# Kernel tuning notes

Measured on AMD Instinct MI355X. Metric: run time of the kernel, lower is better.

## Reference

```python
import jax, jax.numpy as jnp
import numpy as np

B, H, P, L = 16, 128, 64, 8192  # batch, d_input, d_state, seq_len
TWO_PI = 6.283185307179586


def setup_inputs() -> dict:
    key = jax.random.key(0)
    k_u, k_lr, k_li, k_br, k_bi, k_cr, k_ci, k_d = jax.random.split(key, 8)
    u = jax.random.normal(k_u, (B, H, L), dtype=jnp.float32)
    # continuous-time diagonal state matrix: Lambda = -rand + i*2*pi*rand
    lam_re = -jax.random.uniform(k_lr, (P,), dtype=jnp.float32)
    lam_im = TWO_PI * jax.random.uniform(k_li, (P,), dtype=jnp.float32)
    Lam = lam_re + 1j * lam_im                       # (P,) complex64
    Lambda_bar = jnp.exp(Lam)                        # ZOH with Delta=1
    # continuous B, then ZOH: B_bar = (Lambda_bar - 1)/Lambda * B
    Bc = (jax.random.normal(k_br, (P, H), dtype=jnp.float32)
          + 1j * jax.random.normal(k_bi, (P, H), dtype=jnp.float32))
    B_bar = ((Lambda_bar - 1.0) / Lam)[:, None] * Bc  # (P,H) complex64
    C = (jax.random.normal(k_cr, (H, P), dtype=jnp.float32)
         + 1j * jax.random.normal(k_ci, (H, P), dtype=jnp.float32))
    D = jax.random.normal(k_d, (H, H), dtype=jnp.float32)
    return {
        "u": u,
        "Lambda_re": jnp.real(Lambda_bar).astype(jnp.float32),
        "Lambda_im": jnp.imag(Lambda_bar).astype(jnp.float32),
        "B_re": jnp.real(B_bar).astype(jnp.float32),
        "B_im": jnp.imag(B_bar).astype(jnp.float32),
        "C_re": jnp.real(C).astype(jnp.float32),
        "C_im": jnp.imag(C).astype(jnp.float32),
        "D": D,
    }


def _binary_op(elem_i, elem_j):
    # diagonal linear recurrence combine: (A^i, Bu_i) o (A^j, Bu_j)
    a_i, bu_i = elem_i
    a_j, bu_j = elem_j
    return a_j * a_i, a_j * bu_i + bu_j


def reference(u, Lambda_re, Lambda_im, B_re, B_im, C_re, C_im, D):
    Lambda_bar = Lambda_re + 1j * Lambda_im           # (P,)
    B_bar = B_re + 1j * B_im                          # (P,H)
    C = C_re + 1j * C_im                              # (H,P)
    uc = u.astype(B_bar.dtype)                        # (B,H,L) complex
    Bu = jnp.einsum('ph,bhl->bpl', B_bar, uc)         # (B,P,L)
    A = jnp.broadcast_to(Lambda_bar[None, :, None], Bu.shape)
    # parallel associative scan of the diagonal linear recurrence over L
    _, xs = jax.lax.associative_scan(_binary_op, (A, Bu), axis=2)  # (B,P,L)
    C_A_Bu = jnp.einsum('hp,bpl->bhl', C, xs).real    # (B,H,L)
    # einsum('hh,bhl->bhl', D, u) uses only the diagonal of D
    Du = jnp.diagonal(D)[None, :, None] * u           # (B,H,L)
    return jax.nn.gelu(C_A_Bu + Du, approximate=False)
```

## Files before the change

### kernel.cpp

```cpp
#include <hip/hip_runtime.h>
#include <math.h>

#define NB 16
#define NH 128
#define NP 64
#define NL 8192
#define NCHUNK 64

__global__ __launch_bounds__(256) void k_bu_scan(
    const float* __restrict__ u, const float* __restrict__ Bre,
    const float* __restrict__ Bim, const float* __restrict__ Lre,
    const float* __restrict__ Lim, float2* __restrict__ xloc,
    float2* __restrict__ Echunk) {
  __shared__ __align__(16) float sBre[32][68];
  __shared__ float sBim[32][68];
  __shared__ float sU[32][128];
  const int b  = blockIdx.y;
  const int c  = blockIdx.x;
  const int l0 = c * 128;
  const int t  = threadIdx.x;
  const int tp = t & 15;
  const int tl = t >> 4;
  float accRe[4][8], accIm[4][8];
  #pragma unroll
  for (int i = 0; i < 4; ++i)
    #pragma unroll
    for (int j = 0; j < 8; ++j) { accRe[i][j] = 0.f; accIm[i][j] = 0.f; }

  for (int ht = 0; ht < 4; ++ht) {
    const int h0 = ht * 32;
    #pragma unroll
    for (int idx = t; idx < 2048; idx += 256) {
      int h = idx & 31, p = idx >> 5;
      sBre[h][p] = Bre[p * NH + h0 + h];
      sBim[h][p] = Bim[p * NH + h0 + h];
    }
    #pragma unroll
    for (int idx = t; idx < 32 * 128; idx += 256) {
      int l = idx & 127, h = idx >> 7;
      sU[h][l] = u[((size_t)(b * NH + h0 + h)) * NL + l0 + l];
    }
    __syncthreads();
    #pragma unroll 4
    for (int h = 0; h < 32; ++h) {
      float4 br4 = *(const float4*)&sBre[h][tp * 4];
      float4 bi4 = *(const float4*)&sBim[h][tp * 4];
      float4 ua  = *(const float4*)&sU[h][tl * 8];
      float4 ub  = *(const float4*)&sU[h][tl * 8 + 4];
      float uu[8] = {ua.x, ua.y, ua.z, ua.w, ub.x, ub.y, ub.z, ub.w};
      float brr[4] = {br4.x, br4.y, br4.z, br4.w};
      float bii[4] = {bi4.x, bi4.y, bi4.z, bi4.w};
      #pragma unroll
      for (int i = 0; i < 4; ++i)
        #pragma unroll
        for (int j = 0; j < 8; ++j) {
          accRe[i][j] = fmaf(brr[i], uu[j], accRe[i][j]);
          accIm[i][j] = fmaf(bii[i], uu[j], accIm[i][j]);
        }
    }
    __syncthreads();
  }

  float lr[4], li[4];
  #pragma unroll
  for (int i = 0; i < 4; ++i) { lr[i] = Lre[tp * 4 + i]; li[i] = Lim[tp * 4 + i]; }
  #pragma unroll
  for (int i = 0; i < 4; ++i) {
    float xr = 0.f, xi = 0.f;
    #pragma unroll
    for (int j = 0; j < 8; ++j) {
      float nr = fmaf(lr[i], xr, fmaf(-li[i], xi, accRe[i][j]));
      float ni = fmaf(lr[i], xi, fmaf( li[i], xr, accIm[i][j]));
      xr = nr; xi = ni; accRe[i][j] = xr; accIm[i][j] = xi;
    }
  }

  float2* E = reinterpret_cast<float2*>(&sBre[0][0]);
  #define EL(p, q) E[(p) * 17 + (q)]
  #pragma unroll
  for (int i = 0; i < 4; ++i)
    EL(tp * 4 + i, tl) = make_float2(accRe[i][7], accIm[i][7]);

  float wr[4], wi[4];
  #pragma unroll
  for (int i = 0; i < 4; ++i) {
    float ar = lr[i], ai = li[i];
    #pragma unroll
    for (int k = 0; k < 3; ++k) { float nr = ar * ar - ai * ai; ai = 2.f * ar * ai; ar = nr; }
    wr[i] = ar; wi[i] = ai;
  }
  __syncthreads();
  #pragma unroll
  for (int d = 1; d < 16; d <<= 1) {
    float2 rv[4];
    #pragma unroll
    for (int i = 0; i < 4; ++i)
      rv[i] = (tl >= d) ? EL(tp * 4 + i, tl - d) : make_float2(0.f, 0.f);
    __syncthreads();
    if (tl >= d) {
      #pragma unroll
      for (int i = 0; i < 4; ++i) {
        float2 cur = EL(tp * 4 + i, tl);
        cur.x += wr[i] * rv[i].x - wi[i] * rv[i].y;
        cur.y += wr[i] * rv[i].y + wi[i] * rv[i].x;
        EL(tp * 4 + i, tl) = cur;
      }
    }
    __syncthreads();
    #pragma unroll
    for (int i = 0; i < 4; ++i) {
      float nr = wr[i] * wr[i] - wi[i] * wi[i];
      wi[i] = 2.f * wr[i] * wi[i]; wr[i] = nr;
    }
  }

  float2 cin[4];
  #pragma unroll
  for (int i = 0; i < 4; ++i)
    cin[i] = (tl > 0) ? EL(tp * 4 + i, tl - 1) : make_float2(0.f, 0.f);
  if (t < 64) {
    float2 tot = EL(t, 15);
    Echunk[((size_t)(b * NCHUNK + c)) * NP + t] = tot;
  }

  #pragma unroll
  for (int i = 0; i < 4; ++i) {
    float cr = cin[i].x, ci = cin[i].y;
    #pragma unroll
    for (int j = 0; j < 8; ++j) {
      float nr = lr[i] * cr - li[i] * ci;
      float nc = lr[i] * ci + li[i] * cr;
      cr = nr; ci = nc;
      accRe[i][j] += cr; accIm[i][j] += ci;
    }
  }

  #pragma unroll
  for (int i = 0; i < 4; ++i) {
    size_t base = ((size_t)(b * NP + tp * 4 + i)) * NL + l0 + tl * 8;
    #pragma unroll
    for (int j = 0; j < 8; j += 2) {
      float4 v = make_float4(accRe[i][j], accIm[i][j], accRe[i][j + 1], accIm[i][j + 1]);
      *(float4*)&xloc[base + j] = v;
    }
  }
  #undef EL
}

__global__ __launch_bounds__(64) void k_carry(
    const float2* __restrict__ Echunk, const float* __restrict__ Lre,
    const float* __restrict__ Lim, float2* __restrict__ carryg,
    float2* __restrict__ powtab) {
  const int p = blockIdx.x;
  const int b = blockIdx.y;
  const int t = threadIdx.x;
  const float lr = Lre[p], li = Lim[p];
  float wr = lr, wi = li;
  #pragma unroll
  for (int k = 0; k < 7; ++k) { float nr = wr * wr - wi * wi; wi = 2.f * wr * wi; wr = nr; }
  float2 e = Echunk[((size_t)(b * NCHUNK + t)) * NP + p];
  float sr = e.x, si = e.y;
  float fr = wr, fi = wi;
  #pragma unroll
  for (int d = 1; d < 64; d <<= 1) {
    float pr = __shfl_up(sr, d);
    float pi = __shfl_up(si, d);
    if (t >= d) { sr += fr * pr - fi * pi; si += fr * pi + fi * pr; }
    float nr = fr * fr - fi * fi; fi = 2.f * fr * fi; fr = nr;
  }
  float cr = __shfl_up(sr, 1);
  float ci = __shfl_up(si, 1);
  if (t == 0) { cr = 0.f; ci = 0.f; }
  carryg[((size_t)(b * NCHUNK + t)) * NP + p] = make_float2(cr, ci);

  if (b == 0) {
    float ar = lr, ai = li, br = 1.f, bi = 0.f;
    int e1 = t + 1;
    while (e1) {
      if (e1 & 1) { float nr = br * ar - bi * ai; bi = br * ai + bi * ar; br = nr; }
      float nr = ar * ar - ai * ai; ai = 2.f * ar * ai; ar = nr;
      e1 >>= 1;
    }
    powtab[p * 128 + t] = make_float2(br, bi);
    float qr = lr, qi = li;
    #pragma unroll
    for (int k = 0; k < 6; ++k) { float nr = qr * qr - qi * qi; qi = 2.f * qr * qi; qr = nr; }
    float hr = br * qr - bi * qi, hi = br * qi + bi * qr;
    powtab[p * 128 + t + 64] = make_float2(hr, hi);
  }
}

__global__ __launch_bounds__(256) void k_out(
    const float2* __restrict__ xs, const float* __restrict__ u,
    const float* __restrict__ Cre, const float* __restrict__ Cim,
    const float* __restrict__ D, const float2* __restrict__ carryg,
    const float2* __restrict__ powtab, float* __restrict__ out) {
  __shared__ float sCre[16][132];
  __shared__ float sCim[16][132];
  __shared__ float sXre[16][128];
  __shared__ float sXim[16][128];
  __shared__ float sDd[128];
  const int b  = blockIdx.y;
  const int c  = blockIdx.x;
  const int l0 = c * 128;
  const int t  = threadIdx.x;
  const int lane = t & 63, w = t >> 6;
  const int th = (lane & 7) + 8 * (w & 1);
  const int tl = (lane >> 3) + 8 * (w >> 1);
  const int lfix = t & 127;
  const int ppb  = t >> 7;

  if (t < 128) sDd[t] = D[t * NH + t];

  float acc[8][8];
  #pragma unroll
  for (int i = 0; i < 8; ++i)
    #pragma unroll
    for (int j = 0; j < 8; ++j) acc[i][j] = 0.f;

  float2 gx[8], gp[8], gc[8];
  #pragma unroll
  for (int k = 0; k < 8; ++k) {
    int pp = ppb + 2 * k;
    gx[k] = xs[((size_t)(b * NP + pp)) * NL + l0 + lfix];
    gp[k] = powtab[pp * 128 + lfix];
    gc[k] = carryg[((size_t)(b * NCHUNK + c)) * NP + pp];
  }

  #pragma unroll
  for (int pt = 0; pt < 4; ++pt) {
    const int p0 = pt * 16;
    __syncthreads();
    #pragma unroll
    for (int idx = t; idx < 2048; idx += 256) {
      int pp = idx & 15, h = idx >> 4;
      sCre[pp][h] = Cre[h * NP + p0 + pp];
      sCim[pp][h] = Cim[h * NP + p0 + pp];
    }
    #pragma unroll
    for (int k = 0; k < 8; ++k) {
      int pp = ppb + 2 * k;
      float xr = gx[k].x + gp[k].x * gc[k].x - gp[k].y * gc[k].y;
      float xi = gx[k].y + gp[k].x * gc[k].y + gp[k].y * gc[k].x;
      sXre[pp][lfix] = xr; sXim[pp][lfix] = xi;
    }
    __syncthreads();
    if (pt < 3) {
      const int p1 = (pt + 1) * 16;
      #pragma unroll
      for (int k = 0; k < 8; ++k) {
        int pp = ppb + 2 * k;
        gx[k] = xs[((size_t)(b * NP + p1 + pp)) * NL + l0 + lfix];
        gp[k] = powtab[(p1 + pp) * 128 + lfix];
        gc[k] = carryg[((size_t)(b * NCHUNK + c)) * NP + p1 + pp];
      }
    }
    #pragma unroll 4
    for (int pp = 0; pp < 16; ++pp) {
      float4 ca = *(const float4*)&sCre[pp][th * 8];
      float4 cb = *(const float4*)&sCre[pp][th * 8 + 4];
      float4 ia = *(const float4*)&sCim[pp][th * 8];
      float4 ib = *(const float4*)&sCim[pp][th * 8 + 4];
      float4 xa = *(const float4*)&sXre[pp][tl * 8];
      float4 xb = *(const float4*)&sXre[pp][tl * 8 + 4];
      float4 ya = *(const float4*)&sXim[pp][tl * 8];
      float4 yb = *(const float4*)&sXim[pp][tl * 8 + 4];
      float cr[8] = {ca.x, ca.y, ca.z, ca.w, cb.x, cb.y, cb.z, cb.w};
      float ci[8] = {ia.x, ia.y, ia.z, ia.w, ib.x, ib.y, ib.z, ib.w};
      float xr[8] = {xa.x, xa.y, xa.z, xa.w, xb.x, xb.y, xb.z, xb.w};
      float xi[8] = {ya.x, ya.y, ya.z, ya.w, yb.x, yb.y, yb.z, yb.w};
      #pragma unroll
      for (int i = 0; i < 8; ++i)
        #pragma unroll
        for (int j = 0; j < 8; ++j) {
          acc[i][j] = fmaf(cr[i], xr[j], acc[i][j]);
          acc[i][j] = fmaf(-ci[i], xi[j], acc[i][j]);
        }
    }
  }

  #pragma unroll
  for (int i = 0; i < 8; ++i) {
    const int h = th * 8 + i;
    const float dd = sDd[h];
    size_t rb = ((size_t)(b * NH + h)) * NL + l0 + tl * 8;
    float4 u0 = *(const float4*)&u[rb];
    float4 u1 = *(const float4*)&u[rb + 4];
    float uu[8] = {u0.x, u0.y, u0.z, u0.w, u1.x, u1.y, u1.z, u1.w};
    float r[8];
    #pragma unroll
    for (int j = 0; j < 8; ++j) {
      float vv = acc[i][j] + dd * uu[j];
      r[j] = 0.5f * vv * (1.0f + erff(vv * 0.70710678118654752f));
    }
    *(float4*)&out[rb]     = make_float4(r[0], r[1], r[2], r[3]);
    *(float4*)&out[rb + 4] = make_float4(r[4], r[5], r[6], r[7]);
  }
}

extern "C" void kernel_launch(void* const* d_in, const int* in_sizes, int n_in,
                              void* d_out, int out_size, void* d_ws, size_t ws_size,
                              hipStream_t stream) {
  (void)in_sizes; (void)n_in; (void)out_size; (void)ws_size;
  const float* u   = (const float*)d_in[0];
  const float* Lre = (const float*)d_in[1];
  const float* Lim = (const float*)d_in[2];
  const float* Bre = (const float*)d_in[3];
  const float* Bim = (const float*)d_in[4];
  const float* Cre = (const float*)d_in[5];
  const float* Cim = (const float*)d_in[6];
  const float* Dm  = (const float*)d_in[7];
  float* out = (float*)d_out;

  char* wsb = (char*)d_ws;
  float2* xloc   = (float2*)wsb;
  float2* Echunk = (float2*)(wsb + 67108864);
  float2* carryg = (float2*)(wsb + 67108864 + 524288);
  float2* powtab = (float2*)(wsb + 67108864 + 1048576);

  dim3 g(NL / 128, NB);
  k_bu_scan<<<g, 256, 0, stream>>>(u, Bre, Bim, Lre, Lim, xloc, Echunk);
  dim3 gc(NP, NB);
  k_carry<<<gc, 64, 0, stream>>>(Echunk, Lre, Lim, carryg, powtab);
  k_out<<<g, 256, 0, stream>>>(xloc, u, Cre, Cim, Dm, carryg, powtab, out);
}
```

Baseline: 259.5 us.

## Rewrite output projection kernel with bf16 MFMA and smaller L tiles

Replaces the scalar-FMA complex C·x projection in the output kernel with bf16 MFMA 16x16x32 instructions. C (real and negated imaginary parts) and the carry-corrected states are converted to bf16 and staged in shared memory, and the L tile shrinks to 64 so there are twice as many blocks. The goal is to move the dominant GEMM onto the matrix cores. The cost is lower precision in the projection, plus per-block reconversion of the full C matrix. The epilogue now does scalar, non-vectorised loads of u and stores to out.

```diff
diff --git a/kernel.cpp b/kernel.cpp
--- a/kernel.cpp
+++ b/kernel.cpp
@@ -6,6 +6,13 @@
 #define NP 64
 #define NL 8192
 #define NCHUNK 64
+
+typedef __attribute__((ext_vector_type(8))) short bf16x8;
+typedef __attribute__((ext_vector_type(4))) float f32x4;
+
+__device__ __forceinline__ unsigned toBF(unsigned u) {
+  return (u + 0x7FFFu + ((u >> 16) & 1u)) >> 16;
+}
 
 __global__ __launch_bounds__(256) void k_bu_scan(
     const float* __restrict__ u, const float* __restrict__ Bre,
@@ -190,111 +197,74 @@
   }
 }
 
-__global__ __launch_bounds__(256) void k_out(
+__global__ __launch_bounds__(256) void k_out_mfma(
     const float2* __restrict__ xs, const float* __restrict__ u,
     const float* __restrict__ Cre, const float* __restrict__ Cim,
     const float* __restrict__ D, const float2* __restrict__ carryg,
     const float2* __restrict__ powtab, float* __restrict__ out) {
-  __shared__ float sCre[16][132];
-  __shared__ float sCim[16][132];
-  __shared__ float sXre[16][128];
-  __shared__ float sXim[16][128];
+  __shared__ __align__(16) unsigned short Asl[128][136];
+  __shared__ __align__(16) unsigned short Bsl[64][136];
   __shared__ float sDd[128];
   const int b  = blockIdx.y;
-  const int c  = blockIdx.x;
-  const int l0 = c * 128;
+  const int l0 = blockIdx.x * 64;
   const int t  = threadIdx.x;
   const int lane = t & 63, w = t >> 6;
-  const int th = (lane & 7) + 8 * (w & 1);
-  const int tl = (lane >> 3) + 8 * (w >> 1);
-  const int lfix = t & 127;
-  const int ppb  = t >> 7;
 
   if (t < 128) sDd[t] = D[t * NH + t];
 
-  float acc[8][8];
-  #pragma unroll
-  for (int i = 0; i < 8; ++i)
-    #pragma unroll
-    for (int j = 0; j < 8; ++j) acc[i][j] = 0.f;
-
-  float2 gx[8], gp[8], gc[8];
-  #pragma unroll
-  for (int k = 0; k < 8; ++k) {
-    int pp = ppb + 2 * k;
-    gx[k] = xs[((size_t)(b * NP + pp)) * NL + l0 + lfix];
-    gp[k] = powtab[pp * 128 + lfix];
-    gc[k] = carryg[((size_t)(b * NCHUNK + c)) * NP + pp];
-  }
-
-  #pragma unroll
-  for (int pt = 0; pt < 4; ++pt) {
-    const int p0 = pt * 16;
-    __syncthreads();
-    #pragma unroll
-    for (int idx = t; idx < 2048; idx += 256) {
-      int pp = idx & 15, h = idx >> 4;
-      sCre[pp][h] = Cre[h * NP + p0 + pp];
-      sCim[pp][h] = Cim[h * NP + p0 + pp];
-    }
-    #pragma unroll
-    for (int k = 0; k < 8; ++k) {
-      int pp = ppb + 2 * k;
-      float xr = gx[k].x + gp[k].x * gc[k].x - gp[k].y * gc[k].y;
-      float xi = gx[k].y + gp[k].x * gc[k].y + gp[k].y * gc[k].x;
-      sXre[pp][lfix] = xr; sXim[pp][lfix] = xi;
-    }
-    __syncthreads();
-    if (pt < 3) {
-      const int p1 = (pt + 1) * 16;
-      #pragma unroll
-      for (int k = 0; k < 8; ++k) {
-        int pp = ppb + 2 * k;
-        gx[k] = xs[((size_t)(b * NP + p1 + pp)) * NL + l0 + lfix];
-        gp[k] = powtab[(p1 + pp) * 128 + lfix];
-        gc[k] = carryg[((size_t)(b * NCHUNK + c)) * NP + p1 + pp];
-      }
-    }
-    #pragma unroll 4
-    for (int pp = 0; pp < 16; ++pp) {
-      float4 ca = *(const float4*)&sCre[pp][th * 8];
-      float4 cb = *(const float4*)&sCre[pp][th * 8 + 4];
-      float4 ia = *(const float4*)&sCim[pp][th * 8];
-      float4 ib = *(const float4*)&sCim[pp][th * 8 + 4];
-      float4 xa = *(const float4*)&sXre[pp][tl * 8];
-      float4 xb = *(const float4*)&sXre[pp][tl * 8 + 4];
-      float4 ya = *(const float4*)&sXim[pp][tl * 8];
-      float4 yb = *(const float4*)&sXim[pp][tl * 8 + 4];
-      float cr[8] = {ca.x, ca.y, ca.z, ca.w, cb.x, cb.y, cb.z, cb.w};
-      float ci[8] = {ia.x, ia.y, ia.z, ia.w, ib.x, ib.y, ib.z, ib.w};
-      float xr[8] = {xa.x, xa.y, xa.z, xa.w, xb.x, xb.y, xb.z, xb.w};
-      float xi[8] = {ya.x, ya.y, ya.z, ya.w, yb.x, yb.y, yb.z, yb.w};
-      #pragma unroll
-      for (int i = 0; i < 8; ++i)
-        #pragma unroll
-        for (int j = 0; j < 8; ++j) {
-          acc[i][j] = fmaf(cr[i], xr[j], acc[i][j]);
-          acc[i][j] = fmaf(-ci[i], xi[j], acc[i][j]);
-        }
-    }
-  }
-
-  #pragma unroll
-  for (int i = 0; i < 8; ++i) {
-    const int h = th * 8 + i;
-    const float dd = sDd[h];
-    size_t rb = ((size_t)(b * NH + h)) * NL + l0 + tl * 8;
-    float4 u0 = *(const float4*)&u[rb];
-    float4 u1 = *(const float4*)&u[rb + 4];
-    float uu[8] = {u0.x, u0.y, u0.z, u0.w, u1.x, u1.y, u1.z, u1.w};
-    float r[8];
-    #pragma unroll
-    for (int j = 0; j < 8; ++j) {
-      float vv = acc[i][j] + dd * uu[j];
-      r[j] = 0.5f * vv * (1.0f + erff(vv * 0.70710678118654752f));
-    }
-    *(float4*)&out[rb]     = make_float4(r[0], r[1], r[2], r[3]);
-    *(float4*)&out[rb + 4] = make_float4(r[4], r[5], r[6], r[7]);
+  for (int idx = t; idx < NH * NP; idx += 256) {
+    int h = idx >> 6, p = idx & 63;
+    Asl[h][p]      = (unsigned short)toBF(__float_as_uint(Cre[h * NP + p]));
+    Asl[h][64 + p] = (unsigned short)toBF(__float_as_uint(-Cim[h * NP + p]));
+  }
+
+  {
+    const int l  = t & 63, pb = t >> 6;
+    const int c  = l0 >> 7;
+    const int jj = (l0 & 127) + l;
+    #pragma unroll
+    for (int i = 0; i < 16; ++i) {
+      int p = pb * 16 + i;
+      float2 gx = xs[((size_t)(b * NP + p)) * NL + l0 + l];
+      float2 gp = powtab[p * 128 + jj];
+      float2 gc = carryg[((size_t)(b * NCHUNK + c)) * NP + p];
+      float xr = gx.x + gp.x * gc.x - gp.y * gc.y;
+      float xi = gx.y + gp.x * gc.y + gp.y * gc.x;
+      Bsl[l][p]      = (unsigned short)toBF(__float_as_uint(xr));
+      Bsl[l][64 + p] = (unsigned short)toBF(__float_as_uint(xi));
+    }
+  }
+  __syncthreads();
+
+  const int r16 = lane & 15, kq = lane >> 4;
+  f32x4 acc[8];
+  #pragma unroll
+  for (int mt = 0; mt < 8; ++mt) acc[mt] = (f32x4){0.f, 0.f, 0.f, 0.f};
+
+  bf16x8 bfr[4];
+  #pragma unroll
+  for (int kt = 0; kt < 4; ++kt)
+    bfr[kt] = *(const bf16x8*)&Bsl[w * 16 + r16][kt * 32 + kq * 8];
+
+  #pragma unroll
+  for (int mt = 0; mt < 8; ++mt) {
+    #pragma unroll
+    for (int kt = 0; kt < 4; ++kt) {
+      bf16x8 a = *(const bf16x8*)&Asl[mt * 16 + r16][kt * 32 + kq * 8];
+      acc[mt] = __builtin_amdgcn_mfma_f32_16x16x32_bf16(a, bfr[kt], acc[mt], 0, 0, 0);
+    }
+  }
+
+  const int lcol = l0 + w * 16 + r16;
+  #pragma unroll
+  for (int mt = 0; mt < 8; ++mt) {
+    #pragma unroll
+    for (int r = 0; r < 4; ++r) {
+      int h = mt * 16 + kq * 4 + r;
+      size_t o = ((size_t)(b * NH + h)) * NL + lcol;
+      float vv = acc[mt][r] + sDd[h] * u[o];
+      out[o] = 0.5f * vv * (1.0f + erff(vv * 0.70710678118654752f));
+    }
   }
 }
 
@@ -318,9 +288,10 @@
   float2* carryg = (float2*)(wsb + 67108864 + 524288);
   float2* powtab = (float2*)(wsb + 67108864 + 1048576);
 
-  dim3 g(NL / 128, NB);
-  k_bu_scan<<<g, 256, 0, stream>>>(u, Bre, Bim, Lre, Lim, xloc, Echunk);
+  dim3 g1(NL / 128, NB);
+  k_bu_scan<<<g1, 256, 0, stream>>>(u, Bre, Bim, Lre, Lim, xloc, Echunk);
   dim3 gc(NP, NB);
   k_carry<<<gc, 64, 0, stream>>>(Echunk, Lre, Lim, carryg, powtab);
-  k_out<<<g, 256, 0, stream>>>(xloc, u, Cre, Cim, Dm, carryg, powtab, out);
-}
+  dim3 g3(NL / 64, NB);
+  k_out_mfma<<<g3, 256, 0, stream>>>(xloc, u, Cre, Cim, Dm, carryg, powtab, out);
+}
```

Result: faster. 251.0 us (-3.2%).
